# Kernel optimization log

Measured on AMD Instinct MI355X. Metric: run time of the kernel, lower is better.

## Reference

```python
import jax, jax.numpy as jnp
from jax import lax
import numpy as np

B, T, D, H = 64, 512, 1024, 1024

def _xavier(key, shape):
    fan_out, fan_in = shape
    limit = float(np.sqrt(6.0 / (fan_in + fan_out)))
    return jax.random.uniform(key, shape, jnp.float32, -limit, limit)

def setup_inputs() -> dict:
    key = jax.random.key(0)
    ks = jax.random.split(key, 12)
    inp = {
        "input_seq": jax.random.normal(ks[0], (B, T, D), jnp.float32),
        "h_0": jax.random.normal(ks[1], (B, H), jnp.float32),
        "c_0": jax.random.normal(ks[2], (B, H), jnp.float32),
        "W_ii": _xavier(ks[3], (H, D)),
        "W_hi": _xavier(ks[4], (H, H)),
        "b_i": jnp.zeros((H,), jnp.float32),
        "W_if": _xavier(ks[5], (H, D)),
        "W_hf": _xavier(ks[6], (H, H)),
        "b_f": jnp.zeros((H,), jnp.float32),
        "W_ig": _xavier(ks[7], (H, D)),
        "W_hg": _xavier(ks[8], (H, H)),
        "b_g": jnp.zeros((H,), jnp.float32),
        "W_io": _xavier(ks[9], (H, D)),
        "W_ho": _xavier(ks[10], (H, H)),
        "b_o": jnp.zeros((H,), jnp.float32),
    }
    return inp

def reference(input_seq, h_0, c_0, W_ii, W_hi, b_i, W_if, W_hf, b_f,
              W_ig, W_hg, b_g, W_io, W_ho, b_o):
    # Fuse the 4 input-to-hidden projections into one big GEMM over the whole
    # sequence (same math as per-step x_t @ W.T), and the 4 hidden-to-hidden
    # projections into one GEMM inside the scan step.
    Wi = jnp.concatenate([W_ii, W_if, W_ig, W_io], axis=0)  # [4H, D]
    Wh = jnp.concatenate([W_hi, W_hf, W_hg, W_ho], axis=0)  # [4H, H]
    b = jnp.concatenate([b_i, b_f, b_g, b_o])               # [4H]
    x_proj = jnp.einsum('btd,gd->btg', input_seq, Wi) + b   # [B, T, 4H]

    def step(carry, xp_t):
        h, c = carry
        gates = xp_t + h @ Wh.T                              # [B, 4H]
        i, f, g, o = jnp.split(gates, 4, axis=-1)
        i = jax.nn.sigmoid(i)
        f = jax.nn.sigmoid(f)
        g = jnp.tanh(g)
        o = jax.nn.sigmoid(o)
        c = f * c + i * g
        h = o * jnp.tanh(c)
        return (h, c), h

    (h_t, c_t), hs = lax.scan(step, (h_0, c_0), jnp.swapaxes(x_proj, 0, 1))
    h_seq = jnp.swapaxes(hs, 0, 1)  # [B, T, H]
    return h_seq, (h_t, c_t)
```

## Files before the change

### kernel.cpp

```cpp
#include <hip/hip_runtime.h>
#include <cstdint>
#include <cstdio>


typedef _Float16 half8 __attribute__((ext_vector_type(8)));
typedef _Float16 half4 __attribute__((ext_vector_type(4)));
typedef float f32x4 __attribute__((ext_vector_type(4)));

typedef __attribute__((address_space(1))) uint32_t gu32;
typedef __attribute__((address_space(3))) uint32_t lu32;

#define MFMA16(a, b, c) __builtin_amdgcn_mfma_f32_16x16x32_f16((a), (b), (c), 0, 0, 0)

#define XP_OFF   0ull
#define AH_OFF   268435456ull
#define WI_OFF   335544320ull
#define WH_OFF   343932928ull
#define HBF_OFF  352321536ull
#define CNT_OFF  352583680ull
#define WS_NEED  352584704ull

#define RED_STRIDE 66

__device__ inline float sigmoid_f(float x) { return 1.f / (1.f + __expf(-x)); }
__device__ inline float tanh_f(float x) {
  float ax = fabsf(x);
  float e = __expf(-2.f * ax);
  float t = (1.f - e) / (1.f + e);
  return x < 0.f ? -t : t;
}

__global__ void k_init(const float* __restrict__ h0, _Float16* __restrict__ hbf,
                       int* __restrict__ cnt) {
  int i = blockIdx.x * 256 + threadIdx.x;
  hbf[i] = (_Float16)h0[i];
  if (blockIdx.x == 0) cnt[threadIdx.x] = 0;
}

__global__ void k_castx(const float* __restrict__ x, _Float16* __restrict__ xh) {
  size_t i = ((size_t)blockIdx.x * 256 + threadIdx.x) * 8;
  float4 a = *(const float4*)(x + i);
  float4 b = *(const float4*)(x + i + 4);
  half8 o = {(_Float16)a.x, (_Float16)a.y, (_Float16)a.z, (_Float16)a.w,
             (_Float16)b.x, (_Float16)b.y, (_Float16)b.z, (_Float16)b.w};
  *(half8*)(xh + i) = o;
}

__global__ void k_weights(const float* __restrict__ Wii, const float* __restrict__ Wif,
                          const float* __restrict__ Wig, const float* __restrict__ Wio,
                          const float* __restrict__ Whi, const float* __restrict__ Whf,
                          const float* __restrict__ Whg, const float* __restrict__ Who,
                          _Float16* __restrict__ WI, _Float16* __restrict__ WH) {
  int r = blockIdx.x;
  int p = r & 4095;
  int nb = p >> 6, gi = (p >> 4) & 3, uu = p & 15;
  int srow = nb * 16 + uu;
  const float* src;
  if (r < 4096) src = (gi == 0 ? Wii : gi == 1 ? Wif : gi == 2 ? Wig : Wio);
  else          src = (gi == 0 ? Whi : gi == 1 ? Whf : gi == 2 ? Whg : Who);
  src += (size_t)srow * 1024;
  _Float16* dst = (r < 4096 ? WI : WH) + (size_t)p * 1024;
  int c = threadIdx.x * 4;
  float4 v = *(const float4*)(src + c);
  half4 o = {(_Float16)v.x, (_Float16)v.y, (_Float16)v.z, (_Float16)v.w};
  *(half4*)(dst + c) = o;
}

__global__ __launch_bounds__(256) void k_gemm(const _Float16* __restrict__ A,
                                              const _Float16* __restrict__ B,
                                              _Float16* __restrict__ XPo) {
  __shared__ __align__(16) _Float16 As[128 * 32];
  __shared__ __align__(16) _Float16 Bs[128 * 32];
  const int tid = threadIdx.x;
  const int w = tid >> 6, l = tid & 63;
  const int wm = w >> 1, wn = w & 1;
  const int lm = l & 15, lq = l >> 4;
  const size_t m0 = (size_t)blockIdx.x * 128;
  const size_t n0 = (size_t)blockIdx.y * 128;

  f32x4 acc[4][4] = {};

  const int r0 = tid >> 2, c0_ = tid & 3;
  const int r1 = (256 + tid) >> 2, c1_ = tid & 3;
  const _Float16* ga0 = A + (m0 + r0) * 1024 + c0_ * 8;
  const _Float16* ga1 = A + (m0 + r1) * 1024 + c1_ * 8;
  const _Float16* gb0 = B + (n0 + r0) * 1024 + c0_ * 8;
  const _Float16* gb1 = B + (n0 + r1) * 1024 + c1_ * 8;
  _Float16* laBase = As + (size_t)w * 512;
  _Float16* lbBase = Bs + (size_t)w * 512;

  for (int kt = 0; kt < 32; ++kt) {
    const int k0 = kt * 32;
    __syncthreads();
    __builtin_amdgcn_global_load_lds((gu32*)(ga0 + k0), (lu32*)laBase, 16, 0, 0);
    __builtin_amdgcn_global_load_lds((gu32*)(ga1 + k0), (lu32*)(laBase + 2048), 16, 0, 0);
    __builtin_amdgcn_global_load_lds((gu32*)(gb0 + k0), (lu32*)lbBase, 16, 0, 0);
    __builtin_amdgcn_global_load_lds((gu32*)(gb1 + k0), (lu32*)(lbBase + 2048), 16, 0, 0);
    __syncthreads();

    half8 af[4], bf[4];
#pragma unroll
    for (int mi = 0; mi < 4; ++mi)
      af[mi] = *(const half8*)(As + (size_t)(wm * 64 + mi * 16 + lm) * 32 + lq * 8);
#pragma unroll
    for (int ni = 0; ni < 4; ++ni)
      bf[ni] = *(const half8*)(Bs + (size_t)(wn * 64 + ni * 16 + lm) * 32 + lq * 8);
#pragma unroll
    for (int mi = 0; mi < 4; ++mi)
#pragma unroll
      for (int ni = 0; ni < 4; ++ni)
        acc[mi][ni] = MFMA16(af[mi], bf[ni], acc[mi][ni]);
  }

#pragma unroll
  for (int mi = 0; mi < 4; ++mi) {
#pragma unroll
    for (int r = 0; r < 4; ++r) {
      size_t m = m0 + wm * 64 + mi * 16 + lq * 4 + r;
      _Float16* orow = XPo + m * 4096 + n0 + wn * 64 + lm;
#pragma unroll
      for (int ni = 0; ni < 4; ++ni) orow[ni * 16] = (_Float16)acc[mi][ni][r];
    }
  }
}

__global__ __launch_bounds__(256, 1) void k_rnn(
    const _Float16* __restrict__ XP, const _Float16* __restrict__ WH,
    const float* __restrict__ c0,
    const float* __restrict__ bI, const float* __restrict__ bF,
    const float* __restrict__ bG, const float* __restrict__ bO,
    _Float16* __restrict__ hbf, int* __restrict__ cnt, float* __restrict__ out) {
  __shared__ __align__(16) char smem[131072 + RED_STRIDE * 64 * 4];
  _Float16* wl = (_Float16*)smem;
  float* red = (float*)(smem + 131072);

  const int tid = threadIdx.x;
  const int mb = blockIdx.x & 3;
  const int nb = blockIdx.x >> 2;

  const _Float16* wsrc = WH + (size_t)nb * 64 * 1024;
#pragma unroll 4
  for (int it = 0; it < 32; ++it) {
    int s = it * 256 + tid;
    int row = s & 63, kc = s >> 6;
    *(half8*)(wl + (size_t)s * 8) = *(const half8*)(wsrc + (size_t)row * 1024 + kc * 8);
  }

  const int w = tid >> 6, l = tid & 63;
  const int lm = l & 15, lq = l >> 4;
  const int bl = tid >> 4, uu = tid & 15;
  const int bgrow = mb * 16 + bl;
  const int u = nb * 16 + uu;

  float c = c0[(size_t)bgrow * 1024 + u];
  const float bias0 = bI[u], bias1 = bF[u], bias2 = bG[u], bias3 = bO[u];
  const size_t xpth = (size_t)bgrow * 512 * 4096 + (size_t)nb * 64 + uu;
  int* mycnt = cnt + mb * 64;

  const size_t habase = (size_t)(mb * 16 + lm) * 1024 + (size_t)lq * 8 + (size_t)w * 256;

  float xn0 = (float)XP[xpth];
  float xn1 = (float)XP[xpth + 16];
  float xn2 = (float)XP[xpth + 32];
  float xn3 = (float)XP[xpth + 48];

  __syncthreads();

  for (int t = 0; t < 512; ++t) {
    const float xv0 = xn0, xv1 = xn1, xv2 = xn2, xv3 = xn3;

    const uint64_t* hq =
        (const uint64_t*)(hbf + (size_t)(t & 1) * 65536 + habase);
    uint64_t hraw[16];
#pragma unroll
    for (int kk = 0; kk < 8; ++kk) {
      hraw[2 * kk] = __hip_atomic_load(hq + (size_t)kk * 8, __ATOMIC_RELAXED,
                                       __HIP_MEMORY_SCOPE_AGENT);
      hraw[2 * kk + 1] = __hip_atomic_load(hq + (size_t)kk * 8 + 1, __ATOMIC_RELAXED,
                                           __HIP_MEMORY_SCOPE_AGENT);
    }

    f32x4 a0 = {0.f, 0.f, 0.f, 0.f}, a1 = a0, a2 = a0, a3 = a0;
#pragma unroll
    for (int kk = 0; kk < 8; ++kk) {
      union { uint64_t q[2]; half8 v; } av_;
      av_.q[0] = hraw[2 * kk];
      av_.q[1] = hraw[2 * kk + 1];
      const int k0 = w * 256 + kk * 32;
      const _Float16* bb = wl + (size_t)(k0 / 8 + lq) * 512 + lm * 8;
      a0 = MFMA16(av_.v, *(const half8*)(bb), a0);
      a1 = MFMA16(av_.v, *(const half8*)(bb + 128), a1);
      a2 = MFMA16(av_.v, *(const half8*)(bb + 256), a2);
      a3 = MFMA16(av_.v, *(const half8*)(bb + 384), a3);
    }
#pragma unroll
    for (int r = 0; r < 4; ++r) {
      float* rr = red + (size_t)(w * 16 + lq * 4 + r) * RED_STRIDE + lm;
      rr[0] = a0[r]; rr[16] = a1[r]; rr[32] = a2[r]; rr[48] = a3[r];
    }
    __syncthreads();

    float p0 = xv0 + bias0, p1 = xv1 + bias1, p2 = xv2 + bias2, p3 = xv3 + bias3;
#pragma unroll
    for (int ww = 0; ww < 4; ++ww) {
      const float* rr = red + (size_t)(ww * 16 + bl) * RED_STRIDE + uu;
      p0 += rr[0]; p1 += rr[16]; p2 += rr[32]; p3 += rr[48];
    }
    float ig = sigmoid_f(p0), fg = sigmoid_f(p1), gg = tanh_f(p2), og = sigmoid_f(p3);
    c = fg * c + ig * gg;
    float h = og * tanh_f(c);

    out[(size_t)(bgrow * 512 + t) * 1024 + u] = h;

    uint32_t hbits = (uint32_t)__builtin_bit_cast(unsigned short, (_Float16)h);
    uint32_t other = (uint32_t)__shfl_xor((int)hbits, 1, 64);
    if ((uu & 1) == 0) {
      uint32_t packed = hbits | (other << 16);
      uint32_t* hx = (uint32_t*)(hbf + (size_t)((t + 1) & 1) * 65536);
      __hip_atomic_store(hx + ((size_t)bgrow * 1024 + u) / 2, packed,
                         __ATOMIC_RELAXED, __HIP_MEMORY_SCOPE_AGENT);
    }
    if (t == 511) {
      out[33554432u + (size_t)bgrow * 1024 + u] = h;
      out[33554432u + 65536u + (size_t)bgrow * 1024 + u] = c;
    }

    if (t < 511) {
      const size_t xb = xpth + (size_t)(t + 1) * 4096;
      xn0 = (float)XP[xb];
      xn1 = (float)XP[xb + 16];
      xn2 = (float)XP[xb + 32];
      xn3 = (float)XP[xb + 48];
    }

    asm volatile("s_waitcnt vmcnt(0)" ::: "memory");
    __syncthreads();
    if (tid == 0) {
      __hip_atomic_fetch_add(mycnt, 1, __ATOMIC_RELAXED, __HIP_MEMORY_SCOPE_AGENT);
      const int target = 64 * (t + 1);
      while (__hip_atomic_load(mycnt, __ATOMIC_RELAXED, __HIP_MEMORY_SCOPE_AGENT) <
             target) {
        __builtin_amdgcn_s_sleep(1);
      }
    }
    __syncthreads();
  }
}

extern "C" void kernel_launch(void* const* d_in, const int* in_sizes, int n_in,
                              void* d_out, int out_size, void* d_ws, size_t ws_size,
                              hipStream_t stream) {
  const float* x   = (const float*)d_in[0];
  const float* h0  = (const float*)d_in[1];
  const float* c0  = (const float*)d_in[2];
  const float* Wii = (const float*)d_in[3];
  const float* Whi = (const float*)d_in[4];
  const float* bI  = (const float*)d_in[5];
  const float* Wif = (const float*)d_in[6];
  const float* Whf = (const float*)d_in[7];
  const float* bF  = (const float*)d_in[8];
  const float* Wig = (const float*)d_in[9];
  const float* Whg = (const float*)d_in[10];
  const float* bG  = (const float*)d_in[11];
  const float* Wio = (const float*)d_in[12];
  const float* Who = (const float*)d_in[13];
  const float* bO  = (const float*)d_in[14];
  float* out = (float*)d_out;

  if (ws_size < WS_NEED) {
    fprintf(stderr, "kernel_launch: ws too small (%zu < %llu)\n", ws_size,
            (unsigned long long)WS_NEED);
    return;
  }
  char* ws = (char*)d_ws;
  _Float16* XP  = (_Float16*)(ws + XP_OFF);
  _Float16* AH  = (_Float16*)(ws + AH_OFF);
  _Float16* WI  = (_Float16*)(ws + WI_OFF);
  _Float16* WH  = (_Float16*)(ws + WH_OFF);
  _Float16* HBF = (_Float16*)(ws + HBF_OFF);
  int* CNT = (int*)(ws + CNT_OFF);

  k_init<<<256, 256, 0, stream>>>(h0, HBF, CNT);
  k_castx<<<16384, 256, 0, stream>>>(x, AH);
  k_weights<<<8192, 256, 0, stream>>>(Wii, Wif, Wig, Wio, Whi, Whf, Whg, Who, WI, WH);
  k_gemm<<<dim3(256, 32), 256, 0, stream>>>(AH, WI, XP);
  k_rnn<<<256, 256, 0, stream>>>(XP, WH, c0, bI, bF, bG, bO, HBF, CNT, out);
}
```

Measured before the change: 3.144 ms.

## Replace atomic counter barrier with per-block flags and interleave gate weight layout

Each step's grid-wide barrier changes from a shared fetch-add counter polled by one thread with sleep to per-block flag stores, with all 64 lanes of every wave polling the 64 peer flags via __any. The weight rows are reordered so the four gates of each unit sit next to each other. This lets the x-projection be read as a single half4 and the LDS reduction as float4 loads (RED_STRIDE goes to 68 for alignment). The output store and the next x-projection load now happen after the flag is published, overlapping the wait. The risk is more polling traffic from every wave, and stale flags if the workspace is not reset between calls.

```diff
diff --git a/kernel.cpp b/kernel.cpp
--- a/kernel.cpp
+++ b/kernel.cpp
@@ -20,7 +20,7 @@
 #define CNT_OFF  352583680ull
 #define WS_NEED  352584704ull
 
-#define RED_STRIDE 66
+#define RED_STRIDE 68
 
 __device__ inline float sigmoid_f(float x) { return 1.f / (1.f + __expf(-x)); }
 __device__ inline float tanh_f(float x) {
@@ -53,7 +53,7 @@
                           _Float16* __restrict__ WI, _Float16* __restrict__ WH) {
   int r = blockIdx.x;
   int p = r & 4095;
-  int nb = p >> 6, gi = (p >> 4) & 3, uu = p & 15;
+  int nb = p >> 6, uu = (p >> 2) & 15, gi = p & 3;
   int srow = nb * 16 + uu;
   const float* src;
   if (r < 4096) src = (gi == 0 ? Wii : gi == 1 ? Wif : gi == 2 ? Wig : Wio);
@@ -154,20 +154,18 @@
 
   float c = c0[(size_t)bgrow * 1024 + u];
   const float bias0 = bI[u], bias1 = bF[u], bias2 = bG[u], bias3 = bO[u];
-  const size_t xpth = (size_t)bgrow * 512 * 4096 + (size_t)nb * 64 + uu;
-  int* mycnt = cnt + mb * 64;
+  const size_t xpth = (size_t)bgrow * 512 * 4096 + (size_t)nb * 64 + (size_t)uu * 4;
+  int* flg = cnt + mb * 64;
 
   const size_t habase = (size_t)(mb * 16 + lm) * 1024 + (size_t)lq * 8 + (size_t)w * 256;
 
-  float xn0 = (float)XP[xpth];
-  float xn1 = (float)XP[xpth + 16];
-  float xn2 = (float)XP[xpth + 32];
-  float xn3 = (float)XP[xpth + 48];
+  half4 xn = *(const half4*)(XP + xpth);
 
   __syncthreads();
 
   for (int t = 0; t < 512; ++t) {
-    const float xv0 = xn0, xv1 = xn1, xv2 = xn2, xv3 = xn3;
+    const float xv0 = (float)xn[0], xv1 = (float)xn[1];
+    const float xv2 = (float)xn[2], xv3 = (float)xn[3];
 
     const uint64_t* hq =
         (const uint64_t*)(hbf + (size_t)(t & 1) * 65536 + habase);
@@ -203,47 +201,40 @@
     float p0 = xv0 + bias0, p1 = xv1 + bias1, p2 = xv2 + bias2, p3 = xv3 + bias3;
 #pragma unroll
     for (int ww = 0; ww < 4; ++ww) {
-      const float* rr = red + (size_t)(ww * 16 + bl) * RED_STRIDE + uu;
-      p0 += rr[0]; p1 += rr[16]; p2 += rr[32]; p3 += rr[48];
+      const float4 v = *(const float4*)(red + (size_t)(ww * 16 + bl) * RED_STRIDE + uu * 4);
+      p0 += v.x; p1 += v.y; p2 += v.z; p3 += v.w;
     }
     float ig = sigmoid_f(p0), fg = sigmoid_f(p1), gg = tanh_f(p2), og = sigmoid_f(p3);
     c = fg * c + ig * gg;
     float h = og * tanh_f(c);
 
-    out[(size_t)(bgrow * 512 + t) * 1024 + u] = h;
-
-    uint32_t hbits = (uint32_t)__builtin_bit_cast(unsigned short, (_Float16)h);
-    uint32_t other = (uint32_t)__shfl_xor((int)hbits, 1, 64);
-    if ((uu & 1) == 0) {
-      uint32_t packed = hbits | (other << 16);
-      uint32_t* hx = (uint32_t*)(hbf + (size_t)((t + 1) & 1) * 65536);
-      __hip_atomic_store(hx + ((size_t)bgrow * 1024 + u) / 2, packed,
-                         __ATOMIC_RELAXED, __HIP_MEMORY_SCOPE_AGENT);
-    }
-    if (t == 511) {
+    if (t < 511) {
+      uint32_t hbits = (uint32_t)__builtin_bit_cast(unsigned short, (_Float16)h);
+      uint32_t other = (uint32_t)__shfl_xor((int)hbits, 1, 64);
+      if ((uu & 1) == 0) {
+        uint32_t packed = hbits | (other << 16);
+        uint32_t* hx = (uint32_t*)(hbf + (size_t)((t + 1) & 1) * 65536);
+        __hip_atomic_store(hx + ((size_t)bgrow * 1024 + u) / 2, packed,
+                           __ATOMIC_RELAXED, __HIP_MEMORY_SCOPE_AGENT);
+      }
+      asm volatile("s_waitcnt vmcnt(0)" ::: "memory");
+      __syncthreads();
+      if (tid == 0)
+        __hip_atomic_store(flg + nb, t + 1, __ATOMIC_RELAXED,
+                           __HIP_MEMORY_SCOPE_AGENT);
+
+      out[(size_t)(bgrow * 512 + t) * 1024 + u] = h;
+      xn = *(const half4*)(XP + xpth + (size_t)(t + 1) * 4096);
+
+      int fv;
+      do {
+        fv = __hip_atomic_load(flg + l, __ATOMIC_RELAXED, __HIP_MEMORY_SCOPE_AGENT);
+      } while (__any(fv <= t));
+    } else {
+      out[(size_t)(bgrow * 512 + t) * 1024 + u] = h;
       out[33554432u + (size_t)bgrow * 1024 + u] = h;
       out[33554432u + 65536u + (size_t)bgrow * 1024 + u] = c;
     }
-
-    if (t < 511) {
-      const size_t xb = xpth + (size_t)(t + 1) * 4096;
-      xn0 = (float)XP[xb];
-      xn1 = (float)XP[xb + 16];
-      xn2 = (float)XP[xb + 32];
-      xn3 = (float)XP[xb + 48];
-    }
-
-    asm volatile("s_waitcnt vmcnt(0)" ::: "memory");
-    __syncthreads();
-    if (tid == 0) {
-      __hip_atomic_fetch_add(mycnt, 1, __ATOMIC_RELAXED, __HIP_MEMORY_SCOPE_AGENT);
-      const int target = 64 * (t + 1);
-      while (__hip_atomic_load(mycnt, __ATOMIC_RELAXED, __HIP_MEMORY_SCOPE_AGENT) <
-             target) {
-        __builtin_amdgcn_s_sleep(1);
-      }
-    }
-    __syncthreads();
   }
 }
 
```

New measurement: 3.118 ms. Within noise of the previous version (-0.8%).
